# Optimization experiments

Measured on AMD Instinct MI355X. Metric: run time of the kernel, lower is better.

Reference implementation:

```python
import jax, jax.numpy as jnp
import numpy as np

EPS = 1e-5
H = 128          # hidden_size
IN = 75          # input_size
T = 128          # seq len == window_size
B = 1024
OUT = 256        # lstm_output_size


def _bn(x, gamma, beta):
    # training-mode batch norm over the batch dim (biased variance, as in PyTorch BN)
    m = x.mean(axis=0)
    v = x.var(axis=0)
    return gamma * (x - m) * jax.lax.rsqrt(v + EPS) + beta


def _run_bnlstm_layer(xs, Wih, Whh, b, gih, bih, ghh, bhh, gc, bc):
    # xs: (T, B, D). Returns hidden stream (T, B, H).
    Bsz = xs.shape[1]
    h0 = jnp.zeros((Bsz, H), xs.dtype)
    c0 = jnp.zeros((Bsz, H), xs.dtype)

    def step(carry, x):
        h, c = carry
        gates = _bn(x @ Wih, gih, bih) + _bn(h @ Whh, ghh, bhh) + b  # (B, 4H)
        f, i, o, g = jnp.split(gates, 4, axis=1)                     # gate order f,i,o,g
        c1 = jax.nn.sigmoid(f) * c + jax.nn.sigmoid(i) * jnp.tanh(g)
        h1 = jax.nn.sigmoid(o) * jnp.tanh(_bn(c1, gc, bc))
        return (h1, c1), h1

    (_, _), hs = jax.lax.scan(step, (h0, c0), xs)
    return hs


def setup_inputs() -> dict:
    key = jax.random.key(0)
    ks = jax.random.split(key, 12)
    s = 0.05
    d = {
        'sequences': jax.random.normal(ks[0], (B, T, IN), jnp.float32),
        # layer 0 BNLSTM cell params (weights stored as (in, 4H) so y = x @ W)
        'Wih0': jax.random.normal(ks[1], (IN, 4 * H), jnp.float32) * s,
        'Whh0': jax.random.normal(ks[2], (H, 4 * H), jnp.float32) * s,
        'b0': jnp.zeros((4 * H,), jnp.float32),
        'gih0': jnp.full((4 * H,), 0.1, jnp.float32),
        'bih0': jnp.zeros((4 * H,), jnp.float32),
        'ghh0': jnp.full((4 * H,), 0.1, jnp.float32),
        'bhh0': jnp.zeros((4 * H,), jnp.float32),
        'gc0': jnp.full((H,), 0.1, jnp.float32),
        'bc0': jnp.zeros((H,), jnp.float32),
        # layer 1
        'Wih1': jax.random.normal(ks[3], (H, 4 * H), jnp.float32) * s,
        'Whh1': jax.random.normal(ks[4], (H, 4 * H), jnp.float32) * s,
        'b1': jnp.zeros((4 * H,), jnp.float32),
        'gih1': jnp.full((4 * H,), 0.1, jnp.float32),
        'bih1': jnp.zeros((4 * H,), jnp.float32),
        'ghh1': jnp.full((4 * H,), 0.1, jnp.float32),
        'bhh1': jnp.zeros((4 * H,), jnp.float32),
        'gc1': jnp.full((H,), 0.1, jnp.float32),
        'bc1': jnp.zeros((H,), jnp.float32),
        # fc: hidden -> lstm_output_size; decoder: lstm_output_size -> T*IN
        'fc_w': jax.random.normal(ks[5], (H, OUT), jnp.float32) * s,
        'fc_b': jnp.zeros((OUT,), jnp.float32),
        'dec_w': jax.random.normal(ks[6], (OUT, T * IN), jnp.float32) * s,
        'dec_b': jnp.zeros((T * IN,), jnp.float32),
    }
    return d


def reference(sequences, Wih0, Whh0, b0, gih0, bih0, ghh0, bhh0, gc0, bc0,
              Wih1, Whh1, b1, gih1, bih1, ghh1, bhh1, gc1, bc1,
              fc_w, fc_b, dec_w, dec_b):
    xs = jnp.transpose(sequences, (1, 0, 2))  # (T, B, IN), time-major
    hs0 = _run_bnlstm_layer(xs, Wih0, Whh0, b0, gih0, bih0, ghh0, bhh0, gc0, bc0)
    hs1 = _run_bnlstm_layer(hs0, Wih1, Whh1, b1, gih1, bih1, ghh1, bhh1, gc1, bc1)
    last = hs1[-1]                       # (B, H): last time step of top layer
    emb = last @ fc_w + fc_b             # (B, OUT)
    out = emb @ dec_w + dec_b            # (B, T*IN)
    return out.reshape(-1, T, IN)
```

## Files before the change

### kernel.cpp

```cpp
#include <hip/hip_runtime.h>
#include <stdint.h>
#include <stddef.h>

#define TT   128
#define BB   1024
#define INN  75
#define HH   128
#define KXP  96
#define OUTN 256
#define DECN 9600
#define EPSB 1e-5f

typedef short v8s __attribute__((ext_vector_type(8)));
typedef float v4f __attribute__((ext_vector_type(4)));
typedef unsigned short ush;
typedef unsigned int   u32;
typedef unsigned long long u64;

__device__ __align__(256) ush g_xpad[(size_t)TT * BB * KXP];
__device__ __align__(256) u64 g_G1[(size_t)TT * 32 * BB * 4];
__device__ __align__(256) u64 g_h0s[(size_t)TT * BB * 32];
__device__ __align__(256) u64 g_h1s[(size_t)TT * BB * 32];
__device__ __align__(256) float g_c[(size_t)2 * 32 * BB * 4];
__device__ __align__(256) float g_P[(size_t)3 * 32 * BB * 16];
__device__ __align__(256) float g_pst[32 * 16 * 3 * 16 * 2];
__device__ __align__(256) ush g_wtih0[512 * KXP];
__device__ __align__(256) ush g_wthh0[512 * HH];
__device__ __align__(256) ush g_wtih1[512 * HH];
__device__ __align__(256) ush g_wthh1[512 * HH];
__device__ __align__(256) ush g_fcwt[OUTN * HH];
__device__ __align__(256) ush g_decwt[(size_t)DECN * OUTN];
__device__ __align__(256) ush g_emb[BB * OUTN];

__device__ __forceinline__ ush f2bf(float f) {
  u32 u = __float_as_uint(f);
  u32 r = (u + 0x7FFFu + ((u >> 16) & 1u)) >> 16;
  return (ush)r;
}
__device__ __forceinline__ float bf2f(ush u) { return __uint_as_float(((u32)u) << 16); }
__device__ __forceinline__ float sigf(float x)  { return 1.f / (1.f + __expf(-x)); }
__device__ __forceinline__ float tanhf_(float x){ float e = __expf(2.f * x); return 1.f - 2.f / (e + 1.f); }
__device__ __forceinline__ v8s ld8(const ush* p) { return *reinterpret_cast<const v8s*>(p); }
__device__ __forceinline__ int origcol(int m) { return (m & 3) * 128 + (m >> 4) * 4 + ((m >> 2) & 3); }

__global__ void kpackx(const float* __restrict__ seq) {
  int idx = blockIdx.x * 256 + threadIdx.x;
  int kk = idx % KXP; int rest = idx / KXP;
  int b = rest % BB;  int t = rest / BB;
  float v = (kk < INN) ? seq[((size_t)b * TT + t) * INN + kk] : 0.f;
  g_xpad[idx] = f2bf(v);
}

__global__ void kpackw(const float* __restrict__ Wih0, const float* __restrict__ Whh0,
                       const float* __restrict__ Wih1, const float* __restrict__ Whh1,
                       const float* __restrict__ fcw,  const float* __restrict__ decw) {
  int idx = blockIdx.x * 256 + threadIdx.x;
  if (idx < 49152) {
    int m = idx / KXP, k = idx % KXP;
    g_wtih0[idx] = f2bf((k < INN) ? Wih0[k * 512 + origcol(m)] : 0.f);
  } else if (idx < 114688) {
    int j = idx - 49152; int m = j / HH, k = j % HH;
    g_wthh0[j] = f2bf(Whh0[k * 512 + origcol(m)]);
  } else if (idx < 180224) {
    int j = idx - 114688; int m = j / HH, k = j % HH;
    g_wtih1[j] = f2bf(Wih1[k * 512 + origcol(m)]);
  } else if (idx < 245760) {
    int j = idx - 180224; int m = j / HH, k = j % HH;
    g_wthh1[j] = f2bf(Whh1[k * 512 + origcol(m)]);
  } else if (idx < 278528) {
    int j = idx - 245760; int c = j / HH, k = j % HH;
    g_fcwt[j] = f2bf(fcw[k * OUTN + c]);
  } else {
    int j = idx - 278528; int n = j % DECN, k = j / DECN;
    g_decwt[(size_t)n * OUTN + k] = f2bf(decw[(size_t)k * DECN + n]);
  }
}

__global__ __launch_bounds__(512) void kprep(const float* __restrict__ gih0,
                                             const float* __restrict__ bih0,
                                             const float* __restrict__ b0) {
  const int t = blockIdx.x >> 3, ct = blockIdx.x & 7;
  const int tid = threadIdx.x, wv = tid >> 6, l = tid & 63;
  const int lm = l & 15, lq = l >> 4;
  const int R0 = wv * 128;
  __shared__ float sred[8][64][2];
  __shared__ float scoef[64][2];

  v8s af[4][3];
#pragma unroll
  for (int tt = 0; tt < 4; ++tt)
#pragma unroll
    for (int ks = 0; ks < 3; ++ks)
      af[tt][ks] = ld8(&g_wtih0[(ct * 64 + tt * 16 + lm) * KXP + ks * 32 + lq * 8]);

  const v4f vz = {0.f, 0.f, 0.f, 0.f};
  v4f acc[8][4];
#pragma unroll
  for (int mt = 0; mt < 8; ++mt)
#pragma unroll
    for (int tt = 0; tt < 4; ++tt) acc[mt][tt] = vz;

#pragma unroll
  for (int mt = 0; mt < 8; ++mt) {
    const ush* xr = g_xpad + ((size_t)t * BB + R0 + mt * 16 + lm) * KXP + lq * 8;
    v8s bx0 = ld8(xr), bx1 = ld8(xr + 32), bx2 = ld8(xr + 64);
#pragma unroll
    for (int tt = 0; tt < 4; ++tt) {
      acc[mt][tt] = __builtin_amdgcn_mfma_f32_16x16x32_bf16(af[tt][0], bx0, acc[mt][tt], 0, 0, 0);
      acc[mt][tt] = __builtin_amdgcn_mfma_f32_16x16x32_bf16(af[tt][1], bx1, acc[mt][tt], 0, 0, 0);
      acc[mt][tt] = __builtin_amdgcn_mfma_f32_16x16x32_bf16(af[tt][2], bx2, acc[mt][tt], 0, 0, 0);
    }
  }
  float S[4][4], Q[4][4];
#pragma unroll
  for (int tt = 0; tt < 4; ++tt)
#pragma unroll
    for (int r = 0; r < 4; ++r) {
      float s = 0.f, q = 0.f;
#pragma unroll
      for (int mt = 0; mt < 8; ++mt) { float a = acc[mt][tt][r]; s += a; q += a * a; }
#pragma unroll
      for (int off = 1; off < 16; off <<= 1) { s += __shfl_xor(s, off); q += __shfl_xor(q, off); }
      S[tt][r] = s; Q[tt][r] = q;
    }
  if (lm == 0)
#pragma unroll
    for (int tt = 0; tt < 4; ++tt)
#pragma unroll
      for (int r = 0; r < 4; ++r) {
        sred[wv][tt * 16 + lq * 4 + r][0] = S[tt][r];
        sred[wv][tt * 16 + lq * 4 + r][1] = Q[tt][r];
      }
  __syncthreads();
  if (tid < 64) {
    float Sa = 0.f, Qa = 0.f;
#pragma unroll
    for (int w8 = 0; w8 < 8; ++w8) { Sa += sred[w8][tid][0]; Qa += sred[w8][tid][1]; }
    int oc = origcol(ct * 64 + tid);
    float m_ = Sa * (1.f / BB), v_ = Qa * (1.f / BB) - m_ * m_;
    float A = gih0[oc] * rsqrtf(v_ + EPSB);
    scoef[tid][0] = A; scoef[tid][1] = bih0[oc] - A * m_ + b0[oc];
  }
  __syncthreads();
  float CA[4][4], CD[4][4];
#pragma unroll
  for (int tt = 0; tt < 4; ++tt)
#pragma unroll
    for (int r = 0; r < 4; ++r) {
      CA[tt][r] = scoef[tt * 16 + lq * 4 + r][0];
      CD[tt][r] = scoef[tt * 16 + lq * 4 + r][1];
    }
#pragma unroll
  for (int mt = 0; mt < 8; ++mt) {
    const int row = R0 + mt * 16 + lm;
#pragma unroll
    for (int tt = 0; tt < 4; ++tt) {
      const int g = ct * 4 + tt;
      u32 lo = (u32)f2bf(CA[tt][0] * acc[mt][tt][0] + CD[tt][0])
             | ((u32)f2bf(CA[tt][1] * acc[mt][tt][1] + CD[tt][1]) << 16);
      u32 hi = (u32)f2bf(CA[tt][2] * acc[mt][tt][2] + CD[tt][2])
             | ((u32)f2bf(CA[tt][3] * acc[mt][tt][3] + CD[tt][3]) << 16);
      g_G1[(((size_t)t * 32 + g) * BB + row) * 4 + lq] = (u64)lo | ((u64)hi << 32);
    }
  }
}

__global__ __launch_bounds__(256, 2) void kA(int s) {
  const int tid = threadIdx.x;
  const int wv = tid >> 6, l = tid & 63;
  const int lm = l & 15, lq = l >> 4;
  const int c = blockIdx.x & 31, r16 = blockIdx.x >> 5;
  const int row = r16 * 64 + wv * 16 + lm;

  __shared__ float sred[4][16][6];

  const bool h0ok = (s >= 1), h1ok = (s >= 2);
  const ush* const h0r = reinterpret_cast<const ush*>(g_h0s);
  const ush* const h1r = reinterpret_cast<const ush*>(g_h1s);

  v8s af0[4], af1[4], af2[4];
#pragma unroll
  for (int ks = 0; ks < 4; ++ks) {
    af0[ks] = ld8(&g_wthh0[(c * 16 + lm) * HH + ks * 32 + lq * 8]);
    af1[ks] = ld8(&g_wtih1[(c * 16 + lm) * HH + ks * 32 + lq * 8]);
    af2[ks] = ld8(&g_wthh1[(c * 16 + lm) * HH + ks * 32 + lq * 8]);
  }

  const v4f vz = {0.f, 0.f, 0.f, 0.f};
  v4f P0 = vz, P1 = vz, P2 = vz;

  if (h0ok) {
    const ush* hp = h0r + ((size_t)(s - 1) * BB + row) * HH + lq * 8;
#pragma unroll
    for (int ks = 0; ks < 4; ++ks) {
      v8s b = ld8(hp + ks * 32);
      P0 = __builtin_amdgcn_mfma_f32_16x16x32_bf16(af0[ks], b, P0, 0, 0, 0);
      P1 = __builtin_amdgcn_mfma_f32_16x16x32_bf16(af1[ks], b, P1, 0, 0, 0);
    }
  }
  if (h1ok) {
    const ush* hp = h1r + ((size_t)(s - 2) * BB + row) * HH + lq * 8;
#pragma unroll
    for (int ks = 0; ks < 4; ++ks)
      P2 = __builtin_amdgcn_mfma_f32_16x16x32_bf16(af2[ks], ld8(hp + ks * 32), P2, 0, 0, 0);
  }

  if (s < TT)
    *reinterpret_cast<v4f*>(&g_P[(((size_t)0 * 32 + c) * BB + row) * 16 + lq * 4]) = P0;
  if (s >= 1) {
    *reinterpret_cast<v4f*>(&g_P[(((size_t)1 * 32 + c) * BB + row) * 16 + lq * 4]) = P1;
    *reinterpret_cast<v4f*>(&g_P[(((size_t)2 * 32 + c) * BB + row) * 16 + lq * 4]) = P2;
  }

  float S[3][4], Q[3][4];
#pragma unroll
  for (int r = 0; r < 4; ++r) {
    S[0][r] = P0[r]; Q[0][r] = P0[r] * P0[r];
    S[1][r] = P1[r]; Q[1][r] = P1[r] * P1[r];
    S[2][r] = P2[r]; Q[2][r] = P2[r] * P2[r];
  }
#pragma unroll
  for (int st = 0; st < 3; ++st)
#pragma unroll
    for (int r = 0; r < 4; ++r) {
      float s_ = S[st][r], q_ = Q[st][r];
#pragma unroll
      for (int off = 1; off < 16; off <<= 1) { s_ += __shfl_xor(s_, off); q_ += __shfl_xor(q_, off); }
      S[st][r] = s_; Q[st][r] = q_;
    }
  if (lm == 0)
#pragma unroll
    for (int st = 0; st < 3; ++st)
#pragma unroll
      for (int r = 0; r < 4; ++r) {
        sred[wv][lq * 4 + r][st * 2]     = S[st][r];
        sred[wv][lq * 4 + r][st * 2 + 1] = Q[st][r];
      }
  __syncthreads();
  if (tid < 16) {
#pragma unroll
    for (int st = 0; st < 3; ++st) {
      float Sa = 0.f, Qa = 0.f;
#pragma unroll
      for (int w4 = 0; w4 < 4; ++w4) { Sa += sred[w4][tid][st * 2]; Qa += sred[w4][tid][st * 2 + 1]; }
      int base = (((c * 16 + r16) * 3 + st) * 16 + tid) * 2;
      g_pst[base] = Sa; g_pst[base + 1] = Qa;
    }
  }
}

__global__ __launch_bounds__(512, 2) void kB(
    int s,
    const float* __restrict__ ghh0, const float* __restrict__ bhh0,
    const float* __restrict__ gc0,  const float* __restrict__ bc0,
    const float* __restrict__ gih1, const float* __restrict__ bih1,
    const float* __restrict__ ghh1, const float* __restrict__ bhh1,
    const float* __restrict__ b1,   const float* __restrict__ gc1,
    const float* __restrict__ bc1) {
  const int L = blockIdx.x >> 5, g = blockIdx.x & 31;
  if (L == 0 && s >= TT) return;
  if (L == 1 && s < 1) return;

  const int tid = threadIdx.x;
  const int wv = tid >> 6, l = tid & 63;
  const int uloc = tid & 3;
  const int rgrp = tid >> 2;

  __shared__ float scoef[16][3];
  __shared__ float scred[8][4][2];
  __shared__ float sccoef[4][2];

  if (tid < 16) {
    const int cb = tid;
    const int oc = origcol(g * 16 + cb);
    if (L == 0) {
      float S = 0.f, Q = 0.f;
#pragma unroll
      for (int r16 = 0; r16 < 16; ++r16) {
        int bi = (((g * 16 + r16) * 3 + 0) * 16 + cb) * 2;
        S += g_pst[bi]; Q += g_pst[bi + 1];
      }
      float m_ = S * (1.f / BB), v_ = Q * (1.f / BB) - m_ * m_;
      float Ah = ghh0[oc] * rsqrtf(v_ + EPSB);
      scoef[cb][0] = Ah; scoef[cb][1] = bhh0[oc] - Ah * m_;
    } else {
      float S1 = 0.f, Q1 = 0.f, S2 = 0.f, Q2 = 0.f;
#pragma unroll
      for (int r16 = 0; r16 < 16; ++r16) {
        int b1i = (((g * 16 + r16) * 3 + 1) * 16 + cb) * 2;
        int b2i = (((g * 16 + r16) * 3 + 2) * 16 + cb) * 2;
        S1 += g_pst[b1i]; Q1 += g_pst[b1i + 1];
        S2 += g_pst[b2i]; Q2 += g_pst[b2i + 1];
      }
      float m1 = S1 * (1.f / BB), v1 = Q1 * (1.f / BB) - m1 * m1;
      float Ai = gih1[oc] * rsqrtf(v1 + EPSB);
      float m2 = S2 * (1.f / BB), v2 = Q2 * (1.f / BB) - m2 * m2;
      float Ah = ghh1[oc] * rsqrtf(v2 + EPSB);
      scoef[cb][0] = Ai; scoef[cb][1] = Ah;
      scoef[cb][2] = bih1[oc] - Ai * m1 + bhh1[oc] - Ah * m2 + b1[oc];
    }
  }
  __syncthreads();

  float C0[4], C1[4], C2[4];
#pragma unroll
  for (int r = 0; r < 4; ++r) {
    C0[r] = scoef[uloc * 4 + r][0];
    C1[r] = scoef[uloc * 4 + r][1];
    C2[r] = scoef[uloc * 4 + r][2];
  }

  float* cptr = &g_c[((size_t)(L * 32 + g) * BB) * 4];
  const bool cold0 = (L == 0) ? (s == 0) : (s == 1);
  const float* Pa = &g_P[(((size_t)(L == 0 ? 0 : 1) * 32 + g) * BB) * 16];
  const float* Pb = &g_P[(((size_t)2 * 32 + g) * BB) * 16];
  const u64*   G1p = &g_G1[(((size_t)s * 32 + g) * BB) * 4];

  float cst[8], so[8];
  float cS = 0.f, cQ = 0.f;
#pragma unroll
  for (int i = 0; i < 8; ++i) {
    const int row = rgrp * 8 + i;
    float gf, gi, go, gg;
    v4f pa = *reinterpret_cast<const v4f*>(&Pa[row * 16 + uloc * 4]);
    if (L == 0) {
      u64 g1 = G1p[row * 4 + uloc];
      gf = bf2f((ush)g1)         + C0[0] * pa[0] + C1[0];
      gi = bf2f((ush)(g1 >> 16)) + C0[1] * pa[1] + C1[1];
      go = bf2f((ush)(g1 >> 32)) + C0[2] * pa[2] + C1[2];
      gg = bf2f((ush)(g1 >> 48)) + C0[3] * pa[3] + C1[3];
    } else {
      v4f pb = *reinterpret_cast<const v4f*>(&Pb[row * 16 + uloc * 4]);
      gf = C0[0] * pa[0] + C1[0] * pb[0] + C2[0];
      gi = C0[1] * pa[1] + C1[1] * pb[1] + C2[1];
      go = C0[2] * pa[2] + C1[2] * pb[2] + C2[2];
      gg = C0[3] * pa[3] + C1[3] * pb[3] + C2[3];
    }
    float cold = cold0 ? 0.f : cptr[row * 4 + uloc];
    float c1 = sigf(gf) * cold + sigf(gi) * tanhf_(gg);
    cst[i] = c1; so[i] = sigf(go);
    cptr[row * 4 + uloc] = c1;
    cS += c1; cQ += c1 * c1;
  }

#pragma unroll
  for (int off = 4; off < 64; off <<= 1) { cS += __shfl_xor(cS, off); cQ += __shfl_xor(cQ, off); }
  if (l < 4) { scred[wv][l][0] = cS; scred[wv][l][1] = cQ; }
  __syncthreads();
  if (tid < 4) {
    float S = 0.f, Q = 0.f;
#pragma unroll
    for (int w8 = 0; w8 < 8; ++w8) { S += scred[w8][tid][0]; Q += scred[w8][tid][1]; }
    float m_ = S * (1.f / BB), v_ = Q * (1.f / BB) - m_ * m_;
    int uu = g * 4 + tid;
    float gcv = (L == 0) ? gc0[uu] : gc1[uu];
    float bcv = (L == 0) ? bc0[uu] : bc1[uu];
    float ac = gcv * rsqrtf(v_ + EPSB);
    sccoef[tid][0] = ac; sccoef[tid][1] = bcv - ac * m_;
  }
  __syncthreads();
  const float ac = sccoef[uloc][0], dc = sccoef[uloc][1];

  u64* hdst = (L == 0) ? &g_h0s[(size_t)s * BB * 32] : &g_h1s[(size_t)(s - 1) * BB * 32];
#pragma unroll
  for (int i = 0; i < 8; ++i) {
    const int row = rgrp * 8 + i;
    u32 v = (u32)f2bf(so[i] * tanhf_(ac * cst[i] + dc));
    u32 a = v | (__shfl_xor(v, 1) << 16);
    u32 b = __shfl_xor(a, 2);
    if (uloc == 0) hdst[(size_t)row * 32 + g] = (u64)a | ((u64)b << 32);
  }
}

__global__ __launch_bounds__(256) void kfc(const float* __restrict__ fcb) {
  const int tid = threadIdx.x, w = tid >> 6, l = tid & 63;
  const int lm = l & 15, lq = l >> 4;
  const int col = blockIdx.x * 16 + lm;
  const ush* hsrc = reinterpret_cast<const ush*>(g_h1s) + (size_t)(TT - 1) * BB * HH;
  v8s bf[4];
#pragma unroll
  for (int ks = 0; ks < 4; ++ks) bf[ks] = ld8(&g_fcwt[col * HH + ks * 32 + lq * 8]);
  const float bias = fcb[col];
  const v4f vz = {0.f, 0.f, 0.f, 0.f};
#pragma unroll
  for (int mt = 0; mt < 16; ++mt) {
    const int rowa = w * 256 + mt * 16 + lm;
    const ush* ap = hsrc + (size_t)rowa * HH + lq * 8;
    v4f acc = vz;
#pragma unroll
    for (int ks = 0; ks < 4; ++ks)
      acc = __builtin_amdgcn_mfma_f32_16x16x32_bf16(ld8(ap + ks * 32), bf[ks], acc, 0, 0, 0);
#pragma unroll
    for (int r = 0; r < 4; ++r) {
      int row = w * 256 + mt * 16 + lq * 4 + r;
      g_emb[row * OUTN + col] = f2bf(acc[r] + bias);
    }
  }
}

__global__ __launch_bounds__(256) void kdec(const float* __restrict__ decb, float* __restrict__ out) {
  const int tid = threadIdx.x, wv = tid >> 6, l = tid & 63;
  const int lm = l & 15, lq = l >> 4;
  const int c0 = blockIdx.x * 16;
  const int R0 = wv * 256;
  v8s af[8];
#pragma unroll
  for (int ks = 0; ks < 8; ++ks) af[ks] = ld8(&g_decwt[(size_t)(c0 + lm) * OUTN + ks * 32 + lq * 8]);
  float bias[4];
#pragma unroll
  for (int r = 0; r < 4; ++r) bias[r] = decb[c0 + lq * 4 + r];
  const v4f vz = {0.f, 0.f, 0.f, 0.f};
#pragma unroll
  for (int mt = 0; mt < 16; ++mt) {
    const int row = R0 + mt * 16 + lm;
    const ush* bp = g_emb + (size_t)row * OUTN + lq * 8;
    v4f acc = vz;
#pragma unroll
    for (int ks = 0; ks < 8; ++ks)
      acc = __builtin_amdgcn_mfma_f32_16x16x32_bf16(af[ks], ld8(bp + ks * 32), acc, 0, 0, 0);
    v4f o;
#pragma unroll
    for (int r = 0; r < 4; ++r) o[r] = acc[r] + bias[r];
    *reinterpret_cast<v4f*>(&out[(size_t)row * DECN + c0 + lq * 4]) = o;
  }
}

extern "C" void kernel_launch(void* const* d_in, const int* in_sizes, int n_in,
                              void* d_out, int out_size, void* d_ws, size_t ws_size,
                              hipStream_t stream) {
  const float* seq  = (const float*)d_in[0];
  const float* Wih0 = (const float*)d_in[1];
  const float* Whh0 = (const float*)d_in[2];
  const float* b0   = (const float*)d_in[3];
  const float* gih0 = (const float*)d_in[4];
  const float* bih0 = (const float*)d_in[5];
  const float* ghh0 = (const float*)d_in[6];
  const float* bhh0 = (const float*)d_in[7];
  const float* gc0  = (const float*)d_in[8];
  const float* bc0  = (const float*)d_in[9];
  const float* Wih1 = (const float*)d_in[10];
  const float* Whh1 = (const float*)d_in[11];
  const float* b1   = (const float*)d_in[12];
  const float* gih1 = (const float*)d_in[13];
  const float* bih1 = (const float*)d_in[14];
  const float* ghh1 = (const float*)d_in[15];
  const float* bhh1 = (const float*)d_in[16];
  const float* gc1  = (const float*)d_in[17];
  const float* bc1  = (const float*)d_in[18];
  const float* fcw  = (const float*)d_in[19];
  const float* fcb  = (const float*)d_in[20];
  const float* decw = (const float*)d_in[21];
  const float* decb = (const float*)d_in[22];
  float* out = (float*)d_out;
  (void)in_sizes; (void)n_in; (void)out_size; (void)d_ws; (void)ws_size;

  kpackx<<<dim3((TT * BB * KXP) / 256), dim3(256), 0, stream>>>(seq);
  kpackw<<<dim3(10688), dim3(256), 0, stream>>>(Wih0, Whh0, Wih1, Whh1, fcw, decw);
  kprep<<<dim3(TT * 8), dim3(512), 0, stream>>>(gih0, bih0, b0);
  for (int s = 0; s <= TT; ++s) {
    kA<<<dim3(512), dim3(256), 0, stream>>>(s);
    kB<<<dim3(64), dim3(512), 0, stream>>>(s, ghh0, bhh0, gc0, bc0,
                                           gih1, bih1, ghh1, bhh1, b1, gc1, bc1);
  }
  kfc<<<dim3(16), dim3(256), 0, stream>>>(fcb);
  kdec<<<dim3(600), dim3(256), 0, stream>>>(decb, out);
}
```

Baseline: 2.715 ms.

## Fuse per-step recurrence kernels into one persistent kernel with a grid barrier

Replaces the 258 per-timestep kA/kB launches with a single persistent 64-block kernel that loops over time steps and synchronizes through a flag-based grid barrier in global memory. Each block now computes its own recurrent matmuls and batch-norm statistics for its gate columns over all 1024 rows. It keeps the cell state in registers, which removes the g_P, g_pst and g_c round trips. This cuts launch overhead and intermediate global traffic. In exchange the matmul work is spread over only 64 blocks instead of 512, and correctness depends on all blocks being co-resident for the spin barrier.

```diff
diff --git a/kernel.cpp b/kernel.cpp
--- a/kernel.cpp
+++ b/kernel.cpp
@@ -10,6 +10,7 @@
 #define OUTN 256
 #define DECN 9600
 #define EPSB 1e-5f
+#define NBLK 64
 
 typedef short v8s __attribute__((ext_vector_type(8)));
 typedef float v4f __attribute__((ext_vector_type(4)));
@@ -21,9 +22,6 @@
 __device__ __align__(256) u64 g_G1[(size_t)TT * 32 * BB * 4];
 __device__ __align__(256) u64 g_h0s[(size_t)TT * BB * 32];
 __device__ __align__(256) u64 g_h1s[(size_t)TT * BB * 32];
-__device__ __align__(256) float g_c[(size_t)2 * 32 * BB * 4];
-__device__ __align__(256) float g_P[(size_t)3 * 32 * BB * 16];
-__device__ __align__(256) float g_pst[32 * 16 * 3 * 16 * 2];
 __device__ __align__(256) ush g_wtih0[512 * KXP];
 __device__ __align__(256) ush g_wthh0[512 * HH];
 __device__ __align__(256) ush g_wtih1[512 * HH];
@@ -31,6 +29,8 @@
 __device__ __align__(256) ush g_fcwt[OUTN * HH];
 __device__ __align__(256) ush g_decwt[(size_t)DECN * OUTN];
 __device__ __align__(256) ush g_emb[BB * OUTN];
+__device__ u32 g_flags[NBLK];
+__device__ u32 g_bgen = 0;
 
 __device__ __forceinline__ ush f2bf(float f) {
   u32 u = __float_as_uint(f);
@@ -42,6 +42,33 @@
 __device__ __forceinline__ float tanhf_(float x){ float e = __expf(2.f * x); return 1.f - 2.f / (e + 1.f); }
 __device__ __forceinline__ v8s ld8(const ush* p) { return *reinterpret_cast<const v8s*>(p); }
 __device__ __forceinline__ int origcol(int m) { return (m & 3) * 128 + (m >> 4) * 4 + ((m >> 2) & 3); }
+
+__device__ __forceinline__ void gridbar(u32 target) {
+  __syncthreads();
+  if (threadIdx.x == 0) {
+    __threadfence();
+    __hip_atomic_store(&g_flags[blockIdx.x], target, __ATOMIC_RELEASE, __HIP_MEMORY_SCOPE_AGENT);
+  }
+  if (blockIdx.x == 0) {
+    const int t = threadIdx.x;
+    if (t >= 1 && t < NBLK) {
+      while (__hip_atomic_load(&g_flags[t], __ATOMIC_RELAXED, __HIP_MEMORY_SCOPE_AGENT) < target)
+        __builtin_amdgcn_s_sleep(8);
+    }
+    __syncthreads();
+    if (t == 0) {
+      __hip_atomic_store(&g_bgen, target, __ATOMIC_RELEASE, __HIP_MEMORY_SCOPE_AGENT);
+      __threadfence();
+    }
+  } else {
+    if (threadIdx.x == 0) {
+      while (__hip_atomic_load(&g_bgen, __ATOMIC_RELAXED, __HIP_MEMORY_SCOPE_AGENT) < target)
+        __builtin_amdgcn_s_sleep(8);
+      __threadfence();
+    }
+  }
+  __syncthreads();
+}
 
 __global__ void kpackx(const float* __restrict__ seq) {
   int idx = blockIdx.x * 256 + threadIdx.x;
@@ -165,92 +192,7 @@
   }
 }
 
-__global__ __launch_bounds__(256, 2) void kA(int s) {
-  const int tid = threadIdx.x;
-  const int wv = tid >> 6, l = tid & 63;
-  const int lm = l & 15, lq = l >> 4;
-  const int c = blockIdx.x & 31, r16 = blockIdx.x >> 5;
-  const int row = r16 * 64 + wv * 16 + lm;
-
-  __shared__ float sred[4][16][6];
-
-  const bool h0ok = (s >= 1), h1ok = (s >= 2);
-  const ush* const h0r = reinterpret_cast<const ush*>(g_h0s);
-  const ush* const h1r = reinterpret_cast<const ush*>(g_h1s);
-
-  v8s af0[4], af1[4], af2[4];
-#pragma unroll
-  for (int ks = 0; ks < 4; ++ks) {
-    af0[ks] = ld8(&g_wthh0[(c * 16 + lm) * HH + ks * 32 + lq * 8]);
-    af1[ks] = ld8(&g_wtih1[(c * 16 + lm) * HH + ks * 32 + lq * 8]);
-    af2[ks] = ld8(&g_wthh1[(c * 16 + lm) * HH + ks * 32 + lq * 8]);
-  }
-
-  const v4f vz = {0.f, 0.f, 0.f, 0.f};
-  v4f P0 = vz, P1 = vz, P2 = vz;
-
-  if (h0ok) {
-    const ush* hp = h0r + ((size_t)(s - 1) * BB + row) * HH + lq * 8;
-#pragma unroll
-    for (int ks = 0; ks < 4; ++ks) {
-      v8s b = ld8(hp + ks * 32);
-      P0 = __builtin_amdgcn_mfma_f32_16x16x32_bf16(af0[ks], b, P0, 0, 0, 0);
-      P1 = __builtin_amdgcn_mfma_f32_16x16x32_bf16(af1[ks], b, P1, 0, 0, 0);
-    }
-  }
-  if (h1ok) {
-    const ush* hp = h1r + ((size_t)(s - 2) * BB + row) * HH + lq * 8;
-#pragma unroll
-    for (int ks = 0; ks < 4; ++ks)
-      P2 = __builtin_amdgcn_mfma_f32_16x16x32_bf16(af2[ks], ld8(hp + ks * 32), P2, 0, 0, 0);
-  }
-
-  if (s < TT)
-    *reinterpret_cast<v4f*>(&g_P[(((size_t)0 * 32 + c) * BB + row) * 16 + lq * 4]) = P0;
-  if (s >= 1) {
-    *reinterpret_cast<v4f*>(&g_P[(((size_t)1 * 32 + c) * BB + row) * 16 + lq * 4]) = P1;
-    *reinterpret_cast<v4f*>(&g_P[(((size_t)2 * 32 + c) * BB + row) * 16 + lq * 4]) = P2;
-  }
-
-  float S[3][4], Q[3][4];
-#pragma unroll
-  for (int r = 0; r < 4; ++r) {
-    S[0][r] = P0[r]; Q[0][r] = P0[r] * P0[r];
-    S[1][r] = P1[r]; Q[1][r] = P1[r] * P1[r];
-    S[2][r] = P2[r]; Q[2][r] = P2[r] * P2[r];
-  }
-#pragma unroll
-  for (int st = 0; st < 3; ++st)
-#pragma unroll
-    for (int r = 0; r < 4; ++r) {
-      float s_ = S[st][r], q_ = Q[st][r];
-#pragma unroll
-      for (int off = 1; off < 16; off <<= 1) { s_ += __shfl_xor(s_, off); q_ += __shfl_xor(q_, off); }
-      S[st][r] = s_; Q[st][r] = q_;
-    }
-  if (lm == 0)
-#pragma unroll
-    for (int st = 0; st < 3; ++st)
-#pragma unroll
-      for (int r = 0; r < 4; ++r) {
-        sred[wv][lq * 4 + r][st * 2]     = S[st][r];
-        sred[wv][lq * 4 + r][st * 2 + 1] = Q[st][r];
-      }
-  __syncthreads();
-  if (tid < 16) {
-#pragma unroll
-    for (int st = 0; st < 3; ++st) {
-      float Sa = 0.f, Qa = 0.f;
-#pragma unroll
-      for (int w4 = 0; w4 < 4; ++w4) { Sa += sred[w4][tid][st * 2]; Qa += sred[w4][tid][st * 2 + 1]; }
-      int base = (((c * 16 + r16) * 3 + st) * 16 + tid) * 2;
-      g_pst[base] = Sa; g_pst[base + 1] = Qa;
-    }
-  }
-}
-
-__global__ __launch_bounds__(512, 2) void kB(
-    int s,
+__global__ __launch_bounds__(512, 2) void krec(
     const float* __restrict__ ghh0, const float* __restrict__ bhh0,
     const float* __restrict__ gc0,  const float* __restrict__ bc0,
     const float* __restrict__ gih1, const float* __restrict__ bih1,
@@ -258,117 +200,168 @@
     const float* __restrict__ b1,   const float* __restrict__ gc1,
     const float* __restrict__ bc1) {
   const int L = blockIdx.x >> 5, g = blockIdx.x & 31;
-  if (L == 0 && s >= TT) return;
-  if (L == 1 && s < 1) return;
-
-  const int tid = threadIdx.x;
-  const int wv = tid >> 6, l = tid & 63;
-  const int uloc = tid & 3;
-  const int rgrp = tid >> 2;
-
+  const int tid = threadIdx.x, wv = tid >> 6, l = tid & 63;
+  const int lm = l & 15, lq = l >> 4;
+
+  __shared__ float sred[8][16][4];
   __shared__ float scoef[16][3];
   __shared__ float scred[8][4][2];
   __shared__ float sccoef[4][2];
-
-  if (tid < 16) {
-    const int cb = tid;
-    const int oc = origcol(g * 16 + cb);
-    if (L == 0) {
-      float S = 0.f, Q = 0.f;
-#pragma unroll
-      for (int r16 = 0; r16 < 16; ++r16) {
-        int bi = (((g * 16 + r16) * 3 + 0) * 16 + cb) * 2;
-        S += g_pst[bi]; Q += g_pst[bi + 1];
-      }
-      float m_ = S * (1.f / BB), v_ = Q * (1.f / BB) - m_ * m_;
-      float Ah = ghh0[oc] * rsqrtf(v_ + EPSB);
-      scoef[cb][0] = Ah; scoef[cb][1] = bhh0[oc] - Ah * m_;
-    } else {
-      float S1 = 0.f, Q1 = 0.f, S2 = 0.f, Q2 = 0.f;
-#pragma unroll
-      for (int r16 = 0; r16 < 16; ++r16) {
-        int b1i = (((g * 16 + r16) * 3 + 1) * 16 + cb) * 2;
-        int b2i = (((g * 16 + r16) * 3 + 2) * 16 + cb) * 2;
-        S1 += g_pst[b1i]; Q1 += g_pst[b1i + 1];
-        S2 += g_pst[b2i]; Q2 += g_pst[b2i + 1];
-      }
-      float m1 = S1 * (1.f / BB), v1 = Q1 * (1.f / BB) - m1 * m1;
-      float Ai = gih1[oc] * rsqrtf(v1 + EPSB);
-      float m2 = S2 * (1.f / BB), v2 = Q2 * (1.f / BB) - m2 * m2;
-      float Ah = ghh1[oc] * rsqrtf(v2 + EPSB);
-      scoef[cb][0] = Ai; scoef[cb][1] = Ah;
-      scoef[cb][2] = bih1[oc] - Ai * m1 + bhh1[oc] - Ah * m2 + b1[oc];
-    }
-  }
+  __shared__ u32 sbase;
+
+  if (tid == 0) sbase = __hip_atomic_load(&g_bgen, __ATOMIC_RELAXED, __HIP_MEMORY_SCOPE_AGENT);
   __syncthreads();
-
-  float C0[4], C1[4], C2[4];
-#pragma unroll
-  for (int r = 0; r < 4; ++r) {
-    C0[r] = scoef[uloc * 4 + r][0];
-    C1[r] = scoef[uloc * 4 + r][1];
-    C2[r] = scoef[uloc * 4 + r][2];
-  }
-
-  float* cptr = &g_c[((size_t)(L * 32 + g) * BB) * 4];
-  const bool cold0 = (L == 0) ? (s == 0) : (s == 1);
-  const float* Pa = &g_P[(((size_t)(L == 0 ? 0 : 1) * 32 + g) * BB) * 16];
-  const float* Pb = &g_P[(((size_t)2 * 32 + g) * BB) * 16];
-  const u64*   G1p = &g_G1[(((size_t)s * 32 + g) * BB) * 4];
-
-  float cst[8], so[8];
-  float cS = 0.f, cQ = 0.f;
-#pragma unroll
-  for (int i = 0; i < 8; ++i) {
-    const int row = rgrp * 8 + i;
-    float gf, gi, go, gg;
-    v4f pa = *reinterpret_cast<const v4f*>(&Pa[row * 16 + uloc * 4]);
-    if (L == 0) {
-      u64 g1 = G1p[row * 4 + uloc];
-      gf = bf2f((ush)g1)         + C0[0] * pa[0] + C1[0];
-      gi = bf2f((ush)(g1 >> 16)) + C0[1] * pa[1] + C1[1];
-      go = bf2f((ush)(g1 >> 32)) + C0[2] * pa[2] + C1[2];
-      gg = bf2f((ush)(g1 >> 48)) + C0[3] * pa[3] + C1[3];
-    } else {
-      v4f pb = *reinterpret_cast<const v4f*>(&Pb[row * 16 + uloc * 4]);
-      gf = C0[0] * pa[0] + C1[0] * pb[0] + C2[0];
-      gi = C0[1] * pa[1] + C1[1] * pb[1] + C2[1];
-      go = C0[2] * pa[2] + C1[2] * pb[2] + C2[2];
-      gg = C0[3] * pa[3] + C1[3] * pb[3] + C2[3];
-    }
-    float cold = cold0 ? 0.f : cptr[row * 4 + uloc];
-    float c1 = sigf(gf) * cold + sigf(gi) * tanhf_(gg);
-    cst[i] = c1; so[i] = sigf(go);
-    cptr[row * 4 + uloc] = c1;
-    cS += c1; cQ += c1 * c1;
-  }
-
-#pragma unroll
-  for (int off = 4; off < 64; off <<= 1) { cS += __shfl_xor(cS, off); cQ += __shfl_xor(cQ, off); }
-  if (l < 4) { scred[wv][l][0] = cS; scred[wv][l][1] = cQ; }
-  __syncthreads();
-  if (tid < 4) {
-    float S = 0.f, Q = 0.f;
-#pragma unroll
-    for (int w8 = 0; w8 < 8; ++w8) { S += scred[w8][tid][0]; Q += scred[w8][tid][1]; }
-    float m_ = S * (1.f / BB), v_ = Q * (1.f / BB) - m_ * m_;
-    int uu = g * 4 + tid;
-    float gcv = (L == 0) ? gc0[uu] : gc1[uu];
-    float bcv = (L == 0) ? bc0[uu] : bc1[uu];
-    float ac = gcv * rsqrtf(v_ + EPSB);
-    sccoef[tid][0] = ac; sccoef[tid][1] = bcv - ac * m_;
-  }
-  __syncthreads();
-  const float ac = sccoef[uloc][0], dc = sccoef[uloc][1];
-
-  u64* hdst = (L == 0) ? &g_h0s[(size_t)s * BB * 32] : &g_h1s[(size_t)(s - 1) * BB * 32];
-#pragma unroll
-  for (int i = 0; i < 8; ++i) {
-    const int row = rgrp * 8 + i;
-    u32 v = (u32)f2bf(so[i] * tanhf_(ac * cst[i] + dc));
-    u32 a = v | (__shfl_xor(v, 1) << 16);
-    u32 b = __shfl_xor(a, 2);
-    if (uloc == 0) hdst[(size_t)row * 32 + g] = (u64)a | ((u64)b << 32);
+  const u32 base = sbase;
+
+  v8s afA[4], afB[4];
+  const ush* wA = (L == 0) ? g_wthh0 : g_wtih1;
+#pragma unroll
+  for (int ks = 0; ks < 4; ++ks) {
+    afA[ks] = ld8(&wA[(g * 16 + lm) * HH + ks * 32 + lq * 8]);
+    afB[ks] = ld8(&g_wthh1[(g * 16 + lm) * HH + ks * 32 + lq * 8]);
+  }
+
+  const ush* const h0r = reinterpret_cast<const ush*>(g_h0s);
+  const ush* const h1r = reinterpret_cast<const ush*>(g_h1s);
+  float cst[8];
+  float so_[8];
+
+#pragma unroll 1
+  for (int s = 0; s <= TT; ++s) {
+    const bool act = (L == 0) ? (s < TT) : (s >= 1);
+    if (act) {
+      const v4f vz = {0.f, 0.f, 0.f, 0.f};
+      v4f PA[8], PB[8];
+#pragma unroll
+      for (int mt = 0; mt < 8; ++mt) { PA[mt] = vz; PB[mt] = vz; }
+
+      if ((L == 1) || (s >= 1)) {
+        const ush* hb = h0r + (size_t)(s - 1) * BB * HH;
+#pragma unroll
+        for (int mt = 0; mt < 8; ++mt) {
+          const ush* hp = hb + (size_t)(wv * 128 + mt * 16 + lm) * HH + lq * 8;
+#pragma unroll
+          for (int ks = 0; ks < 4; ++ks)
+            PA[mt] = __builtin_amdgcn_mfma_f32_16x16x32_bf16(afA[ks], ld8(hp + ks * 32), PA[mt], 0, 0, 0);
+        }
+      }
+      if (L == 1 && s >= 2) {
+        const ush* hb = h1r + (size_t)(s - 2) * BB * HH;
+#pragma unroll
+        for (int mt = 0; mt < 8; ++mt) {
+          const ush* hp = hb + (size_t)(wv * 128 + mt * 16 + lm) * HH + lq * 8;
+#pragma unroll
+          for (int ks = 0; ks < 4; ++ks)
+            PB[mt] = __builtin_amdgcn_mfma_f32_16x16x32_bf16(afB[ks], ld8(hp + ks * 32), PB[mt], 0, 0, 0);
+        }
+      }
+
+      float sA[4], qA[4], sB[4], qB[4];
+#pragma unroll
+      for (int r = 0; r < 4; ++r) {
+        float s1 = 0.f, q1 = 0.f, s2 = 0.f, q2 = 0.f;
+#pragma unroll
+        for (int mt = 0; mt < 8; ++mt) {
+          const float a = PA[mt][r]; s1 += a; q1 += a * a;
+          const float b = PB[mt][r]; s2 += b; q2 += b * b;
+        }
+#pragma unroll
+        for (int off = 1; off < 16; off <<= 1) {
+          s1 += __shfl_xor(s1, off); q1 += __shfl_xor(q1, off);
+          s2 += __shfl_xor(s2, off); q2 += __shfl_xor(q2, off);
+        }
+        sA[r] = s1; qA[r] = q1; sB[r] = s2; qB[r] = q2;
+      }
+      if (lm == 0)
+#pragma unroll
+        for (int r = 0; r < 4; ++r) {
+          sred[wv][lq * 4 + r][0] = sA[r]; sred[wv][lq * 4 + r][1] = qA[r];
+          sred[wv][lq * 4 + r][2] = sB[r]; sred[wv][lq * 4 + r][3] = qB[r];
+        }
+      __syncthreads();
+      if (tid < 16) {
+        float S1 = 0.f, Q1 = 0.f, S2 = 0.f, Q2 = 0.f;
+#pragma unroll
+        for (int w = 0; w < 8; ++w) {
+          S1 += sred[w][tid][0]; Q1 += sred[w][tid][1];
+          S2 += sred[w][tid][2]; Q2 += sred[w][tid][3];
+        }
+        const int oc = origcol(g * 16 + tid);
+        if (L == 0) {
+          const float m_ = S1 * (1.f / BB), v_ = Q1 * (1.f / BB) - m_ * m_;
+          const float Ah = ghh0[oc] * rsqrtf(v_ + EPSB);
+          scoef[tid][0] = Ah; scoef[tid][1] = bhh0[oc] - Ah * m_; scoef[tid][2] = 0.f;
+        } else {
+          const float m1 = S1 * (1.f / BB), v1 = Q1 * (1.f / BB) - m1 * m1;
+          const float Ai = gih1[oc] * rsqrtf(v1 + EPSB);
+          const float m2 = S2 * (1.f / BB), v2 = Q2 * (1.f / BB) - m2 * m2;
+          const float Ah = ghh1[oc] * rsqrtf(v2 + EPSB);
+          scoef[tid][0] = Ai; scoef[tid][1] = Ah;
+          scoef[tid][2] = bih1[oc] - Ai * m1 + bhh1[oc] - Ah * m2 + b1[oc];
+        }
+      }
+      __syncthreads();
+      float C0[4], C1a[4], C2[4];
+#pragma unroll
+      for (int r = 0; r < 4; ++r) {
+        C0[r]  = scoef[lq * 4 + r][0];
+        C1a[r] = scoef[lq * 4 + r][1];
+        C2[r]  = scoef[lq * 4 + r][2];
+      }
+
+      const bool first = (L == 0) ? (s == 0) : (s == 1);
+      float cS = 0.f, cQ = 0.f;
+#pragma unroll
+      for (int mt = 0; mt < 8; ++mt) {
+        const int row = wv * 128 + mt * 16 + lm;
+        float gv0, gv1, gv2, gv3;
+        if (L == 0) {
+          const u64 g1 = g_G1[(((size_t)s * 32 + g) * BB + row) * 4 + lq];
+          gv0 = bf2f((ush)g1)         + C0[0] * PA[mt][0] + C1a[0];
+          gv1 = bf2f((ush)(g1 >> 16)) + C0[1] * PA[mt][1] + C1a[1];
+          gv2 = bf2f((ush)(g1 >> 32)) + C0[2] * PA[mt][2] + C1a[2];
+          gv3 = bf2f((ush)(g1 >> 48)) + C0[3] * PA[mt][3] + C1a[3];
+        } else {
+          gv0 = C0[0] * PA[mt][0] + C1a[0] * PB[mt][0] + C2[0];
+          gv1 = C0[1] * PA[mt][1] + C1a[1] * PB[mt][1] + C2[1];
+          gv2 = C0[2] * PA[mt][2] + C1a[2] * PB[mt][2] + C2[2];
+          gv3 = C0[3] * PA[mt][3] + C1a[3] * PB[mt][3] + C2[3];
+        }
+        const float cold = first ? 0.f : cst[mt];
+        const float c1 = sigf(gv0) * cold + sigf(gv1) * tanhf_(gv3);
+        cst[mt] = c1; so_[mt] = sigf(gv2);
+        cS += c1; cQ += c1 * c1;
+      }
+
+#pragma unroll
+      for (int off = 1; off < 16; off <<= 1) { cS += __shfl_xor(cS, off); cQ += __shfl_xor(cQ, off); }
+      if (lm == 0) { scred[wv][lq][0] = cS; scred[wv][lq][1] = cQ; }
+      __syncthreads();
+      if (tid < 4) {
+        float S = 0.f, Q = 0.f;
+#pragma unroll
+        for (int w = 0; w < 8; ++w) { S += scred[w][tid][0]; Q += scred[w][tid][1]; }
+        const float m_ = S * (1.f / BB), v_ = Q * (1.f / BB) - m_ * m_;
+        const int uu = g * 4 + tid;
+        const float gcv = (L == 0) ? gc0[uu] : gc1[uu];
+        const float bcv = (L == 0) ? bc0[uu] : bc1[uu];
+        const float ac = gcv * rsqrtf(v_ + EPSB);
+        sccoef[tid][0] = ac; sccoef[tid][1] = bcv - ac * m_;
+      }
+      __syncthreads();
+      const float ac = sccoef[lq][0], dc = sccoef[lq][1];
+
+      u64* hdst = (L == 0) ? &g_h0s[(size_t)s * BB * 32] : &g_h1s[(size_t)(s - 1) * BB * 32];
+#pragma unroll
+      for (int mt = 0; mt < 8; ++mt) {
+        const int row = wv * 128 + mt * 16 + lm;
+        const u32 v = (u32)f2bf(so_[mt] * tanhf_(ac * cst[mt] + dc));
+        const u32 a = v | (__shfl_xor(v, 16) << 16);
+        const u32 b = __shfl_xor(a, 32);
+        if (lq == 0) hdst[(size_t)row * 32 + g] = (u64)a | ((u64)b << 32);
+      }
+    }
+    if (s < TT) gridbar(base + (u32)s + 1);
   }
 }
 
@@ -457,11 +450,8 @@
   kpackx<<<dim3((TT * BB * KXP) / 256), dim3(256), 0, stream>>>(seq);
   kpackw<<<dim3(10688), dim3(256), 0, stream>>>(Wih0, Whh0, Wih1, Whh1, fcw, decw);
   kprep<<<dim3(TT * 8), dim3(512), 0, stream>>>(gih0, bih0, b0);
-  for (int s = 0; s <= TT; ++s) {
-    kA<<<dim3(512), dim3(256), 0, stream>>>(s);
-    kB<<<dim3(64), dim3(512), 0, stream>>>(s, ghh0, bhh0, gc0, bc0,
-                                           gih1, bih1, ghh1, bhh1, b1, gc1, bc1);
-  }
+  krec<<<dim3(NBLK), dim3(512), 0, stream>>>(ghh0, bhh0, gc0, bc0,
+                                             gih1, bih1, ghh1, bhh1, b1, gc1, bc1);
   kfc<<<dim3(16), dim3(256), 0, stream>>>(fcb);
   kdec<<<dim3(600), dim3(256), 0, stream>>>(decb, out);
 }
```

New measurement: 3.454 ms. 27.2% more time.
